# Kernel optimization log

Hardware: AMD Instinct MI355X
Metric: run time of the kernel (lower is better)

Reference implementation:

```python
import jax, jax.numpy as jnp
import numpy as np

N, K, IN_DIM, OUT_DIM = 131072, 16, 256, 128


def setup_inputs() -> dict:
    key = jax.random.key(0)
    ks = jax.random.split(key, 6)
    s1 = 1.0 / np.sqrt(IN_DIM)
    s2 = 1.0 / np.sqrt(OUT_DIM)
    return {
        "x": jax.random.normal(ks[0], (N, IN_DIM), dtype=jnp.float32),
        "z": jax.random.randint(ks[1], (N,), 0, K, dtype=jnp.int32),
        "W1": jax.random.uniform(ks[2], (K, IN_DIM, OUT_DIM), jnp.float32, -s1, s1),
        "b1": jax.random.uniform(ks[3], (K, OUT_DIM), jnp.float32, -s1, s1),
        "W2": jax.random.uniform(ks[4], (K, OUT_DIM, 2), jnp.float32, -s2, s2),
        "b2": jax.random.uniform(ks[5], (K, 2), jnp.float32, -s2, s2),
    }


def reference(x, z, W1, b1, W2, b2):
    # Per-cluster expert MLP: tokens with z==i go through expert i.
    # Loop over the fixed, small number of experts (k); data dims stay vectorized.
    k = W1.shape[0]
    ri = jnp.zeros((x.shape[0], 2), dtype=x.dtype)
    for i in range(k):
        h = jax.nn.relu(x @ W1[i] + b1[i])          # [N, out_dim]
        logits = h @ W2[i] + b2[i]                  # [N, 2]
        ri = jnp.where((z == i)[:, None], logits, ri)
    # Every z in [0, k) is covered, so every row of ri has been written
    # (matches the torch path where non-empty clusters overwrite -inf).
    return jax.nn.softmax(ri, axis=-1)
```

## Files before the change

### kernel.cpp

```cpp
#include <hip/hip_runtime.h>
#include <hip/hip_bf16.h>

#define KEXP   16
#define IN_DIM 256
#define OUT_DIM 128
#define TILE   128
#define BPE    16

typedef float f32x4 __attribute__((ext_vector_type(4)));
typedef short bf16x8 __attribute__((ext_vector_type(8)));
typedef const unsigned int __attribute__((address_space(1)))* gptr_t;
typedef unsigned int __attribute__((address_space(3)))* lptr_t;

__device__ __forceinline__ ushort f2bf(float f) {
    union { float f; unsigned u; } v; v.f = f;
    return (ushort)((v.u + 0x7fffu + ((v.u >> 16) & 1u)) >> 16);
}

__global__ __launch_bounds__(256) void prep_k(const float* __restrict__ W1,
                                              ushort* __restrict__ w1t,
                                              const int* __restrict__ z,
                                              int* __restrict__ counts, int n) {
    __shared__ float ld[64][65];
    int bid = blockIdx.x, tid = threadIdx.x;
    if (bid < 128) {
        int e = bid >> 3, sub = bid & 7;
        int k0 = (sub & 3) * 64, n0 = (sub >> 2) * 64;
        const float* src = W1 + (long)e * (IN_DIM * OUT_DIM);
        int tr = tid >> 6, tc = tid & 63;
#pragma unroll
        for (int i = 0; i < 16; i++) {
            int row = i * 4 + tr;
            ld[row][tc] = src[(k0 + row) * OUT_DIM + n0 + tc];
        }
        __syncthreads();
        char* dst = (char*)w1t + (long)e * (OUT_DIM * IN_DIM * 2);
#pragma unroll
        for (int i = 0; i < 16; i++) {
            int col = n0 + i * 4 + tr;
            int L = (col * IN_DIM + k0 + tc) * 2;
            int S = L ^ ((col & 7) << 4);
            *(ushort*)(dst + S) = f2bf(ld[tc][i * 4 + tr]);
        }
    } else {
        int* h = (int*)ld;
        if (tid < KEXP) h[tid] = 0;
        __syncthreads();
        for (int i = (bid - 128) * 256 + tid; i < n; i += 256 * 256)
            atomicAdd(&h[z[i]], 1);
        __syncthreads();
        if (tid < KEXP) atomicAdd(&counts[tid], h[tid]);
    }
}

__global__ void scan_k(const int* __restrict__ counts, int* __restrict__ bases) {
    if (threadIdx.x == 0) {
        int acc = 0;
        for (int i = 0; i < KEXP; i++) { bases[i] = acc; acc += counts[i]; }
    }
}

__global__ __launch_bounds__(256) void scatter_k(const int* __restrict__ z,
                                                 const int* __restrict__ bases,
                                                 int* __restrict__ cursors,
                                                 int* __restrict__ perm, int n) {
    __shared__ int lc[KEXP];
    __shared__ int lb[KEXP];
    int tid = threadIdx.x;
    if (tid < KEXP) lc[tid] = 0;
    __syncthreads();
    int i = blockIdx.x * 256 + tid;
    int e = 0, r = 0;
    if (i < n) {
        e = z[i];
        r = atomicAdd(&lc[e], 1);
    }
    __syncthreads();
    if (tid < KEXP && lc[tid] > 0) lb[tid] = atomicAdd(&cursors[tid], lc[tid]);
    __syncthreads();
    if (i < n) perm[bases[e] + lb[e] + r] = i;
}

__global__ __launch_bounds__(512, 2) void mlp_k(
    const float* __restrict__ x, const float* __restrict__ b1,
    const float* __restrict__ W2, const float* __restrict__ b2,
    const int* __restrict__ counts, const int* __restrict__ bases,
    const int* __restrict__ perm, const ushort* __restrict__ w1t,
    float* __restrict__ out) {
    __shared__ char Wl[65536];
    __shared__ char Al[65536];

    int b = blockIdx.x;
    int e = b >> 4, slot = b & 15;
    int cnt = counts[e];
    int pb0 = bases[e];
    int ntiles = (cnt + TILE - 1) / TILE;

    int tid = threadIdx.x;
    int lane = tid & 63, w = tid >> 6;
    int li = lane & 15, q = lane >> 4;

    const char* wsrc = (const char*)w1t + (long)e * (OUT_DIM * IN_DIM * 2);
#pragma unroll
    for (int i = 0; i < 8; i++) {
        int off = w * 8192 + i * 1024;
        __builtin_amdgcn_global_load_lds((gptr_t)(wsrc + off + lane * 16),
                                         (lptr_t)(Wl + off), 16, 0, 0);
    }

    float bbv[8], w2a[8], w2b[8];
#pragma unroll
    for (int nn = 0; nn < 8; nn++) {
        int col = nn * 16 + li;
        bbv[nn] = b1[e * OUT_DIM + col];
        w2a[nn] = W2[(e * OUT_DIM + col) * 2 + 0];
        w2b[nn] = W2[(e * OUT_DIM + col) * 2 + 1];
    }
    float bb0 = b2[e * 2 + 0], bb1 = b2[e * 2 + 1];

    f32x4 av[16];
    int pb_cur = 0, nr_cur = 0;
    if (slot < ntiles) {
        pb_cur = pb0 + slot * TILE;
        nr_cur = cnt - slot * TILE;
        int rr = w * 16 + li;
        int pv = perm[pb_cur + (rr < nr_cur ? rr : nr_cur - 1)];
#pragma unroll
        for (int i = 0; i < 16; i++) {
            int g = __shfl(pv, i, 16);
            av[i] = *(const f32x4*)((const char*)x + (long)g * 1024 + lane * 16);
        }
    }

    for (int t = slot; t < ntiles; t += BPE) {
#pragma unroll
        for (int i = 0; i < 16; i++) {
            int r = w * 16 + i;
            uint2 pk;
            pk.x = (unsigned)f2bf(av[i][0]) | ((unsigned)f2bf(av[i][1]) << 16);
            pk.y = (unsigned)f2bf(av[i][2]) | ((unsigned)f2bf(av[i][3]) << 16);
            *(uint2*)(Al + r * 512 + ((lane * 8) ^ ((r & 7) << 4))) = pk;
        }
        __syncthreads();

        int tn = t + BPE;
        int pb_nx = 0, nr_nx = 0;
        if (tn < ntiles) {
            pb_nx = pb0 + tn * TILE;
            nr_nx = cnt - tn * TILE;
            int rr = w * 16 + li;
            int pv = perm[pb_nx + (rr < nr_nx ? rr : nr_nx - 1)];
#pragma unroll
            for (int i = 0; i < 16; i++) {
                int g = __shfl(pv, i, 16);
                av[i] = *(const f32x4*)((const char*)x + (long)g * 1024 + lane * 16);
            }
        }

        f32x4 acc[8];
#pragma unroll
        for (int nn = 0; nn < 8; nn++) acc[nn] = (f32x4)0.0f;

        int arow = w * 16 + li;
        int aswz = (arow & 7) << 4;
#pragma unroll
        for (int kk = 0; kk < 8; kk++) {
            bf16x8 af = *(const bf16x8*)(Al + arow * 512 + ((kk * 64 + q * 16) ^ aswz));
#pragma unroll
            for (int nn = 0; nn < 8; nn++) {
                int col = nn * 16 + li;
                bf16x8 bf = *(const bf16x8*)(Wl + col * 512 + ((kk * 64 + q * 16) ^ ((col & 7) << 4)));
                acc[nn] = __builtin_amdgcn_mfma_f32_16x16x32_bf16(af, bf, acc[nn], 0, 0, 0);
            }
        }

        float p0[4] = {0.f, 0.f, 0.f, 0.f}, p1[4] = {0.f, 0.f, 0.f, 0.f};
#pragma unroll
        for (int nn = 0; nn < 8; nn++) {
#pragma unroll
            for (int r = 0; r < 4; r++) {
                float h = fmaxf(acc[nn][r] + bbv[nn], 0.0f);
                p0[r] += h * w2a[nn];
                p1[r] += h * w2b[nn];
            }
        }
#pragma unroll
        for (int m = 1; m < 16; m <<= 1)
#pragma unroll
            for (int r = 0; r < 4; r++) {
                p0[r] += __shfl_xor(p0[r], m, 64);
                p1[r] += __shfl_xor(p1[r], m, 64);
            }
        if (li == 0) {
#pragma unroll
            for (int r = 0; r < 4; r++) {
                int mm = w * 16 + q * 4 + r;
                if (mm < nr_cur) {
                    int orig = perm[pb_cur + mm];
                    float l0 = p0[r] + bb0, l1 = p1[r] + bb1;
                    float mx = fmaxf(l0, l1);
                    float e0 = __expf(l0 - mx), e1 = __expf(l1 - mx);
                    float inv = 1.0f / (e0 + e1);
                    *(float2*)(out + (long)orig * 2) = make_float2(e0 * inv, e1 * inv);
                }
            }
        }
        __syncthreads();
        pb_cur = pb_nx;
        nr_cur = nr_nx;
    }
}

extern "C" void kernel_launch(void* const* d_in, const int* in_sizes, int n_in,
                              void* d_out, int out_size, void* d_ws, size_t ws_size,
                              hipStream_t stream) {
    const float* x  = (const float*)d_in[0];
    const int*   z  = (const int*)d_in[1];
    const float* W1 = (const float*)d_in[2];
    const float* b1 = (const float*)d_in[3];
    const float* W2 = (const float*)d_in[4];
    const float* b2 = (const float*)d_in[5];
    float* out = (float*)d_out;
    int n = in_sizes[1];

    int* counts  = (int*)d_ws;
    int* cursors = counts + 16;
    int* basesp  = counts + 32;
    int* perm    = counts + 256;
    ushort* w1t  = (ushort*)((char*)d_ws + 1024 + (size_t)n * 4);

    hipMemsetAsync(counts, 0, 128, stream);
    prep_k<<<384, 256, 0, stream>>>(W1, w1t, z, counts, n);
    scan_k<<<1, 64, 0, stream>>>(counts, basesp);
    scatter_k<<<(n + 255) / 256, 256, 0, stream>>>(z, basesp, cursors, perm, n);
    mlp_k<<<KEXP * BPE, 512, 0, stream>>>(x, b1, W2, b2, counts, basesp, perm, w1t, out);
}
```

Before: 228.7 us.

## Parallelize scan, batch scatter per thread, pre-pack bf16 A tile, relax launch bounds

The single-thread exclusive scan over the expert counts becomes a wavefront shuffle scan. The scatter kernel now handles four elements per thread, so it launches a quarter as many blocks and issues fewer global cursor atomics. In the MLP kernel, the fp32 to bf16 packing of the prefetched x rows moves to the end of the previous iteration and is stored as packed uint2, so the LDS store phase no longer waits on the conversion. Launch bounds change from 2 blocks per CU to 1, which gives the compiler more registers at the cost of possible occupancy loss.

```diff
diff --git a/kernel.cpp b/kernel.cpp
--- a/kernel.cpp
+++ b/kernel.cpp
@@ -54,10 +54,15 @@
 }
 
 __global__ void scan_k(const int* __restrict__ counts, int* __restrict__ bases) {
-    if (threadIdx.x == 0) {
-        int acc = 0;
-        for (int i = 0; i < KEXP; i++) { bases[i] = acc; acc += counts[i]; }
-    }
+    int li = threadIdx.x & 63;
+    int c = (li < KEXP) ? counts[li] : 0;
+    int v = c;
+#pragma unroll
+    for (int d = 1; d < KEXP; d <<= 1) {
+        int t = __shfl_up(v, d, 64);
+        if (li >= d) v += t;
+    }
+    if (li < KEXP) bases[li] = v - c;
 }
 
 __global__ __launch_bounds__(256) void scatter_k(const int* __restrict__ z,
@@ -69,19 +74,27 @@
     int tid = threadIdx.x;
     if (tid < KEXP) lc[tid] = 0;
     __syncthreads();
-    int i = blockIdx.x * 256 + tid;
-    int e = 0, r = 0;
-    if (i < n) {
-        e = z[i];
-        r = atomicAdd(&lc[e], 1);
+    int base = blockIdx.x * 1024 + tid;
+    int e[4], r[4];
+#pragma unroll
+    for (int j = 0; j < 4; j++) {
+        int i = base + j * 256;
+        if (i < n) {
+            e[j] = z[i];
+            r[j] = atomicAdd(&lc[e[j]], 1);
+        } else e[j] = -1;
     }
     __syncthreads();
     if (tid < KEXP && lc[tid] > 0) lb[tid] = atomicAdd(&cursors[tid], lc[tid]);
     __syncthreads();
-    if (i < n) perm[bases[e] + lb[e] + r] = i;
-}
-
-__global__ __launch_bounds__(512, 2) void mlp_k(
+#pragma unroll
+    for (int j = 0; j < 4; j++) {
+        int i = base + j * 256;
+        if (i < n) perm[bases[e[j]] + lb[e[j]] + r[j]] = i;
+    }
+}
+
+__global__ __launch_bounds__(512, 1) void mlp_k(
     const float* __restrict__ x, const float* __restrict__ b1,
     const float* __restrict__ W2, const float* __restrict__ b2,
     const int* __restrict__ counts, const int* __restrict__ bases,
@@ -118,34 +131,39 @@
     }
     float bb0 = b2[e * 2 + 0], bb1 = b2[e * 2 + 1];
 
-    f32x4 av[16];
+    uint2 pk[16];
     int pb_cur = 0, nr_cur = 0;
     if (slot < ntiles) {
         pb_cur = pb0 + slot * TILE;
         nr_cur = cnt - slot * TILE;
         int rr = w * 16 + li;
         int pv = perm[pb_cur + (rr < nr_cur ? rr : nr_cur - 1)];
+        f32x4 av[16];
 #pragma unroll
         for (int i = 0; i < 16; i++) {
             int g = __shfl(pv, i, 16);
             av[i] = *(const f32x4*)((const char*)x + (long)g * 1024 + lane * 16);
         }
+#pragma unroll
+        for (int i = 0; i < 16; i++) {
+            pk[i].x = (unsigned)f2bf(av[i][0]) | ((unsigned)f2bf(av[i][1]) << 16);
+            pk[i].y = (unsigned)f2bf(av[i][2]) | ((unsigned)f2bf(av[i][3]) << 16);
+        }
     }
 
     for (int t = slot; t < ntiles; t += BPE) {
 #pragma unroll
         for (int i = 0; i < 16; i++) {
             int r = w * 16 + i;
-            uint2 pk;
-            pk.x = (unsigned)f2bf(av[i][0]) | ((unsigned)f2bf(av[i][1]) << 16);
-            pk.y = (unsigned)f2bf(av[i][2]) | ((unsigned)f2bf(av[i][3]) << 16);
-            *(uint2*)(Al + r * 512 + ((lane * 8) ^ ((r & 7) << 4))) = pk;
+            *(uint2*)(Al + r * 512 + ((lane * 8) ^ ((r & 7) << 4))) = pk[i];
         }
         __syncthreads();
 
         int tn = t + BPE;
         int pb_nx = 0, nr_nx = 0;
-        if (tn < ntiles) {
+        f32x4 av[16];
+        bool have_nx = (tn < ntiles);
+        if (have_nx) {
             pb_nx = pb0 + tn * TILE;
             nr_nx = cnt - tn * TILE;
             int rr = w * 16 + li;
@@ -203,6 +221,14 @@
                     float inv = 1.0f / (e0 + e1);
                     *(float2*)(out + (long)orig * 2) = make_float2(e0 * inv, e1 * inv);
                 }
+            }
+        }
+
+        if (have_nx) {
+#pragma unroll
+            for (int i = 0; i < 16; i++) {
+                pk[i].x = (unsigned)f2bf(av[i][0]) | ((unsigned)f2bf(av[i][1]) << 16);
+                pk[i].y = (unsigned)f2bf(av[i][2]) | ((unsigned)f2bf(av[i][3]) << 16);
             }
         }
         __syncthreads();
@@ -232,6 +258,6 @@
     hipMemsetAsync(counts, 0, 128, stream);
     prep_k<<<384, 256, 0, stream>>>(W1, w1t, z, counts, n);
     scan_k<<<1, 64, 0, stream>>>(counts, basesp);
-    scatter_k<<<(n + 255) / 256, 256, 0, stream>>>(z, basesp, cursors, perm, n);
+    scatter_k<<<(n + 1023) / 1024, 256, 0, stream>>>(z, basesp, cursors, perm, n);
     mlp_k<<<KEXP * BPE, 512, 0, stream>>>(x, b1, W2, b2, counts, basesp, perm, w1t, out);
 }
```

Result: no change. 224.4 us (-1.9%).
